# Kernel tuning notes

Measured on AMD Instinct MI355X. Metric: run time of the kernel, lower is better.

Reference implementation:

```python
import jax, jax.numpy as jnp
import numpy as np

N = 50000          # nodes
E = 1600000        # edges
F_IN = 128         # node_features
H = 256            # hidden_dim
A = 16             # action_dim
G = 64             # num graphs in batch


def _sage_conv(x, src, dst, Wl, bl, Wr, num_nodes):
    # PyG SAGEConv (aggr='mean'): out = lin_l(mean_{j in N(i)} x_j) + lin_r(x_i)
    msgs = x[src]                                              # [E, F] gather
    agg = jax.ops.segment_sum(msgs, dst, num_segments=num_nodes)
    cnt = jax.ops.segment_sum(jnp.ones((src.shape[0], 1), x.dtype), dst,
                              num_segments=num_nodes)
    mean = agg / jnp.maximum(cnt, 1.0)                         # [N, F]
    return mean @ Wl + bl + x @ Wr


def setup_inputs() -> dict:
    key = jax.random.key(0)
    ks = jax.random.split(key, 16)
    s = lambda k, sh: jax.random.normal(k, sh, dtype=jnp.float32) * (1.0 / np.sqrt(sh[0]))
    inp = {
        "x": jax.random.normal(ks[0], (N, F_IN), dtype=jnp.float32),
        "edge_index": jax.random.randint(ks[1], (2, E), 0, N, dtype=jnp.int32),
        "batch": jnp.sort(jax.random.randint(ks[2], (N,), 0, G, dtype=jnp.int32)),
        # SAGEConv 1
        "Wl1": s(ks[3], (F_IN, H)), "bl1": jnp.zeros((H,), jnp.float32), "Wr1": s(ks[4], (F_IN, H)),
        # SAGEConv 2
        "Wl2": s(ks[5], (H, H)), "bl2": jnp.zeros((H,), jnp.float32), "Wr2": s(ks[6], (H, H)),
        # actor MLP
        "Wa1": s(ks[7], (H, H)), "ba1": jnp.zeros((H,), jnp.float32),
        "Wa2": s(ks[8], (H, A)), "ba2": jnp.zeros((A,), jnp.float32),
        # critic MLP
        "Wc1": s(ks[9], (H, H)), "bc1": jnp.zeros((H,), jnp.float32),
        "Wc2": s(ks[10], (H, 1)), "bc2": jnp.zeros((1,), jnp.float32),
    }
    return inp


def reference(x, edge_index, batch, Wl1, bl1, Wr1, Wl2, bl2, Wr2,
              Wa1, ba1, Wa2, ba2, Wc1, bc1, Wc2, bc2):
    src, dst = edge_index[0], edge_index[1]
    h = jax.nn.relu(_sage_conv(x, src, dst, Wl1, bl1, Wr1, N))
    h = jax.nn.relu(_sage_conv(h, src, dst, Wl2, bl2, Wr2, N))
    # global_mean_pool over graph ids
    pooled = jax.ops.segment_sum(h, batch, num_segments=G)
    gcnt = jax.ops.segment_sum(jnp.ones((N, 1), h.dtype), batch, num_segments=G)
    g = pooled / jnp.maximum(gcnt, 1.0)                        # [G, H]
    mu = jax.nn.relu(g @ Wa1 + ba1) @ Wa2 + ba2                # [G, A]
    value = jax.nn.relu(g @ Wc1 + bc1) @ Wc2 + bc2             # [G, 1]
    return mu, value
```

## Files before the change

kernel.cpp:

```cpp
#include <hip/hip_runtime.h>
#include <hip/hip_bf16.h>
#include <hip/hip_fp8.h>

#define NN 50000
#define NE 1600000
#define FIN 128
#define HH 256
#define GG 64
#define AA 16
#define NB ((NN + 255) / 256)
#define NRANGE 8
#define RSZ (NN / NRANGE)

typedef __attribute__((ext_vector_type(8))) short short8;
typedef __attribute__((ext_vector_type(4))) float f32x4;
typedef __attribute__((ext_vector_type(4))) int   i32x4;
typedef __attribute__((ext_vector_type(4))) uint  u32x4;

static __device__ __forceinline__ ushort f2b(float f) {
    union { __hip_bfloat16 h; ushort u; } v; v.h = __float2bfloat16(f); return v.u;
}
static __device__ __forceinline__ float b2f_lo(uint a) {
    union { float f; uint u; } v; v.u = a << 16; return v.f;
}
template<int SEL>
static __device__ __forceinline__ float f8tof(uint u) {
#if __has_builtin(__builtin_amdgcn_cvt_f32_fp8)
    return __builtin_amdgcn_cvt_f32_fp8(u, SEL);
#else
    union { unsigned char c; __hip_fp8_e4m3 f; } v;
    v.c = (u >> (SEL * 8)) & 0xFF;
    return (float)v.f;
#endif
}
static __device__ __forceinline__ unsigned char ftof8(float f) {
    __hip_fp8_e4m3 v(f);
    return *reinterpret_cast<unsigned char*>(&v);
}

__global__ void k_prep(const float* __restrict__ x, ushort* __restrict__ xb,
                       unsigned char* __restrict__ xf8,
                       const float* __restrict__ Wl1, const float* __restrict__ Wr1,
                       ushort* __restrict__ Wt1,
                       const float* __restrict__ Wl2, const float* __restrict__ Wr2,
                       ushort* __restrict__ Wt2,
                       int* __restrict__ degi, float* __restrict__ gz) {
    int b = blockIdx.x, t = threadIdx.x;
    if (b < 6250) {
        int i = b * 256 + t;
        float4 v = reinterpret_cast<const float4*>(x)[i];
        ushort4 o; o.x = f2b(v.x); o.y = f2b(v.y); o.z = f2b(v.z); o.w = f2b(v.w);
        reinterpret_cast<ushort4*>(xb)[i] = o;
        uchar4 p; p.x = ftof8(v.x); p.y = ftof8(v.y); p.z = ftof8(v.z); p.w = ftof8(v.w);
        reinterpret_cast<uchar4*>(xf8)[i] = p;
    } else if (b < 6506) {
        int i = (b - 6250) * 256 + t;
        int n = i / 256, k = i % 256;
        float v = (k < 128) ? Wl1[k * HH + n] : Wr1[(k - 128) * HH + n];
        Wt1[i] = f2b(v);
    } else if (b < 7018) {
        int i = (b - 6506) * 256 + t;
        int n = i / 512, k = i % 512;
        float v = (k < 256) ? Wl2[k * HH + n] : Wr2[(k - 256) * HH + n];
        Wt2[i] = f2b(v);
    } else if (b < 7214) {
        int i = (b - 7018) * 256 + t;
        if (i < NN) degi[i] = 0;
    } else {
        int i = (b - 7214) * 256 + t;
        if (i < GG + GG * HH) gz[i] = 0.0f;
    }
}

__global__ void k_degi(const int* __restrict__ dst, int* __restrict__ degi) {
    int range = blockIdx.x & 7;
    int i = (blockIdx.x >> 3) * 256 + threadIdx.x;
    if (i >= NE / 4) return;
    i32x4 d = __builtin_nontemporal_load(reinterpret_cast<const i32x4*>(dst) + i);
    int lo = range * RSZ, hi = lo + RSZ;
    if (d.x >= lo && d.x < hi) atomicAdd(&degi[d.x], 1);
    if (d.y >= lo && d.y < hi) atomicAdd(&degi[d.y], 1);
    if (d.z >= lo && d.z < hi) atomicAdd(&degi[d.z], 1);
    if (d.w >= lo && d.w < hi) atomicAdd(&degi[d.w], 1);
}

__global__ void k_gdeg(const int* __restrict__ batch, float* __restrict__ gcnt) {
    __shared__ float h[GG];
    int t = threadIdx.x;
    if (t < GG) h[t] = 0.0f;
    __syncthreads();
    int i = blockIdx.x * 256 + t;
    if (i < NN) atomicAdd(&h[batch[i]], 1.0f);
    __syncthreads();
    if (t < GG && h[t] != 0.0f) atomicAdd(&gcnt[t], h[t]);
}

__global__ void k_scan1(const int* __restrict__ degi, int* __restrict__ blocksum) {
    __shared__ int s[256];
    int t = threadIdx.x, i = blockIdx.x * 256 + t;
    s[t] = i < NN ? degi[i] : 0;
    __syncthreads();
    for (int d = 128; d > 0; d >>= 1) { if (t < d) s[t] += s[t + d]; __syncthreads(); }
    if (t == 0) blocksum[blockIdx.x] = s[0];
}

__global__ void k_scan2(const int* __restrict__ blocksum, int* __restrict__ blockoff) {
    __shared__ int s[256];
    int t = threadIdx.x;
    int v = t < NB ? blocksum[t] : 0;
    s[t] = v; __syncthreads();
    for (int d = 1; d < 256; d <<= 1) {
        int x = t >= d ? s[t - d] : 0; __syncthreads();
        s[t] += x; __syncthreads();
    }
    if (t < NB) blockoff[t] = s[t] - v;
}

__global__ void k_scan3(const int* __restrict__ degi, const int* __restrict__ blockoff,
                        int* __restrict__ offsets, int* __restrict__ cursor) {
    __shared__ int s[256];
    int t = threadIdx.x, i = blockIdx.x * 256 + t;
    int v = i < NN ? degi[i] : 0;
    s[t] = v; __syncthreads();
    for (int d = 1; d < 256; d <<= 1) {
        int x = t >= d ? s[t - d] : 0; __syncthreads();
        s[t] += x; __syncthreads();
    }
    if (i < NN) {
        int off = blockoff[blockIdx.x] + s[t] - v;
        offsets[i] = off;
        cursor[i]  = off;
    }
    if (i == 0) offsets[NN] = NE;
}

__global__ void k_fill(const int* __restrict__ src, const int* __restrict__ dst,
                       int* __restrict__ cursor, ushort* __restrict__ csr16) {
    int range = blockIdx.x & 7;
    int i = (blockIdx.x >> 3) * 256 + threadIdx.x;
    if (i >= NE / 4) return;
    i32x4 d = __builtin_nontemporal_load(reinterpret_cast<const i32x4*>(dst) + i);
    i32x4 s = __builtin_nontemporal_load(reinterpret_cast<const i32x4*>(src) + i);
    int lo = range * RSZ, hi = lo + RSZ;
    if (d.x >= lo && d.x < hi) csr16[atomicAdd(&cursor[d.x], 1)] = (ushort)s.x;
    if (d.y >= lo && d.y < hi) csr16[atomicAdd(&cursor[d.y], 1)] = (ushort)s.y;
    if (d.z >= lo && d.z < hi) csr16[atomicAdd(&cursor[d.z], 1)] = (ushort)s.z;
    if (d.w >= lo && d.w < hi) csr16[atomicAdd(&cursor[d.w], 1)] = (ushort)s.w;
}

template<int C>
__global__ void __launch_bounds__(256) k_gatherf8(
        const int* __restrict__ offsets, const ushort* __restrict__ csr16,
        const unsigned char* __restrict__ feat, ushort* __restrict__ agg) {
    constexpr int V = C / 64;
    int wid = threadIdx.x >> 6, lane = threadIdx.x & 63;
    int node = blockIdx.x * 4 + wid;
    if (node >= NN) return;
    int o0 = offsets[node], o1 = offsets[node + 1];
    const unsigned char* fp = feat + lane * V;
    float acc[V];
#pragma unroll
    for (int i = 0; i < V; i++) acc[i] = 0.0f;

    int t = o0;
    for (; t + 3 < o1; t += 4) {
        int s0 = __builtin_nontemporal_load(csr16 + t);
        int s1 = __builtin_nontemporal_load(csr16 + t + 1);
        int s2 = __builtin_nontemporal_load(csr16 + t + 2);
        int s3 = __builtin_nontemporal_load(csr16 + t + 3);
        if constexpr (V == 2) {
            uint u0 = *(const ushort*)(fp + (size_t)s0 * C);
            uint u1 = *(const ushort*)(fp + (size_t)s1 * C);
            uint u2 = *(const ushort*)(fp + (size_t)s2 * C);
            uint u3 = *(const ushort*)(fp + (size_t)s3 * C);
            acc[0] += (f8tof<0>(u0) + f8tof<0>(u1)) + (f8tof<0>(u2) + f8tof<0>(u3));
            acc[1] += (f8tof<1>(u0) + f8tof<1>(u1)) + (f8tof<1>(u2) + f8tof<1>(u3));
        } else {
            uint u0 = *(const uint*)(fp + (size_t)s0 * C);
            uint u1 = *(const uint*)(fp + (size_t)s1 * C);
            uint u2 = *(const uint*)(fp + (size_t)s2 * C);
            uint u3 = *(const uint*)(fp + (size_t)s3 * C);
            acc[0] += (f8tof<0>(u0) + f8tof<0>(u1)) + (f8tof<0>(u2) + f8tof<0>(u3));
            acc[1] += (f8tof<1>(u0) + f8tof<1>(u1)) + (f8tof<1>(u2) + f8tof<1>(u3));
            acc[2] += (f8tof<2>(u0) + f8tof<2>(u1)) + (f8tof<2>(u2) + f8tof<2>(u3));
            acc[3] += (f8tof<3>(u0) + f8tof<3>(u1)) + (f8tof<3>(u2) + f8tof<3>(u3));
        }
    }
    for (; t < o1; ++t) {
        int s0 = __builtin_nontemporal_load(csr16 + t);
        if constexpr (V == 2) {
            uint u0 = *(const ushort*)(fp + (size_t)s0 * C);
            acc[0] += f8tof<0>(u0); acc[1] += f8tof<1>(u0);
        } else {
            uint u0 = *(const uint*)(fp + (size_t)s0 * C);
            acc[0] += f8tof<0>(u0); acc[1] += f8tof<1>(u0);
            acc[2] += f8tof<2>(u0); acc[3] += f8tof<3>(u0);
        }
    }

    int deg = o1 - o0;
    float r = __builtin_amdgcn_rcpf(deg > 1 ? (float)deg : 1.0f);
    if constexpr (V == 2) {
        uint o = (uint)f2b(acc[0] * r) | ((uint)f2b(acc[1] * r) << 16);
        *(uint*)(agg + (size_t)node * C + lane * 2) = o;
    } else {
        uint2 o;
        o.x = (uint)f2b(acc[0] * r) | ((uint)f2b(acc[1] * r) << 16);
        o.y = (uint)f2b(acc[2] * r) | ((uint)f2b(acc[3] * r) << 16);
        *(uint2*)(agg + (size_t)node * C + lane * 4) = o;
    }
}

template<int K>
__global__ void __launch_bounds__(256) k_sage_mfma(
        const ushort* __restrict__ agg, const ushort* __restrict__ xin,
        const ushort* __restrict__ Wt, const float* __restrict__ bias,
        ushort* __restrict__ outb, unsigned char* __restrict__ out8) {
    constexpr int KH = K / 2;
    constexpr int LDP = 40;
    __shared__ ushort As[128 * LDP];
    __shared__ ushort Bs[256 * LDP];

    const int tid  = threadIdx.x;
    const int lane = tid & 63;
    const int w    = tid >> 6;
    const int base = blockIdx.x * 128;
    const int r    = lane & 15;
    const int kh   = lane >> 4;
    const int wcol = w * 64;

    f32x4 acc[8][4];
#pragma unroll
    for (int m = 0; m < 8; m++)
#pragma unroll
        for (int n = 0; n < 4; n++) acc[m][n] = (f32x4){0.f, 0.f, 0.f, 0.f};

    const int frowA = tid >> 1;
    const int fqA   = tid & 1;
    const int frowB = tid >> 2;
    const int fqB   = tid & 3;
    int fnode = base + frowA; if (fnode >= NN) fnode = 0;

    for (int k0 = 0; k0 < K; k0 += 32) {
        __syncthreads();
        {
            const ushort* srcp = (k0 < KH)
                ? agg + (size_t)fnode * KH + k0 + fqA * 16
                : xin + (size_t)fnode * KH + (k0 - KH) + fqA * 16;
            u32x4 a0 = *(const u32x4*)srcp;
            u32x4 a1 = *(const u32x4*)(srcp + 8);
            *(u32x4*)(&As[frowA * LDP + fqA * 16])     = a0;
            *(u32x4*)(&As[frowA * LDP + fqA * 16 + 8]) = a1;
        }
#pragma unroll
        for (int s = 0; s < 4; s++) {
            int c = frowB + s * 64;
            *(u32x4*)(&Bs[c * LDP + fqB * 8]) =
                *(const u32x4*)(Wt + (size_t)c * K + k0 + fqB * 8);
        }
        __syncthreads();

        short8 av[8], bv[4];
#pragma unroll
        for (int m = 0; m < 8; m++)
            av[m] = *(const short8*)(&As[(m * 16 + r) * LDP + kh * 8]);
#pragma unroll
        for (int n = 0; n < 4; n++)
            bv[n] = *(const short8*)(&Bs[(wcol + n * 16 + r) * LDP + kh * 8]);
#pragma unroll
        for (int m = 0; m < 8; m++)
#pragma unroll
            for (int n = 0; n < 4; n++)
                acc[m][n] = __builtin_amdgcn_mfma_f32_16x16x32_bf16(
                    av[m], bv[n], acc[m][n], 0, 0, 0);
    }

    float bj[4];
#pragma unroll
    for (int n = 0; n < 4; n++) bj[n] = bias[wcol + n * 16 + r];

#pragma unroll
    for (int m = 0; m < 8; m++) {
        int rowbase = base + m * 16 + (lane >> 4) * 4;
#pragma unroll
        for (int reg = 0; reg < 4; reg++) {
            int nd = rowbase + reg;
            if (nd < NN) {
#pragma unroll
                for (int n = 0; n < 4; n++) {
                    float v = acc[m][n][reg] + bj[n];
                    v = v > 0.0f ? v : 0.0f;
                    outb[(size_t)nd * HH + wcol + n * 16 + r] = f2b(v);
                    if (out8) out8[(size_t)nd * HH + wcol + n * 16 + r] = ftof8(v);
                }
            }
        }
    }
}

__global__ void k_pool(const ushort* __restrict__ h, const int* __restrict__ batch,
                       float* __restrict__ gpool) {
    __shared__ int sb[32];
    int j = threadIdx.x;
    int base = blockIdx.x * 32;
    int n = NN - base; if (n > 32) n = 32;
    if (j < n) sb[j] = batch[base + j];
    __syncthreads();
    float acc = 0.0f;
    int cur = sb[0];
    for (int t = 0; t < n; t++) {
        int g = sb[t];
        if (g != cur) {
            atomicAdd(&gpool[cur * HH + j], acc);
            acc = 0.0f;
            cur = g;
        }
        acc += b2f_lo((uint)h[(size_t)(base + t) * HH + j]);
    }
    atomicAdd(&gpool[cur * HH + j], acc);
}

__global__ void k_head(const float* __restrict__ gpool, const float* __restrict__ gcnt,
                       const float* __restrict__ Wa1, const float* __restrict__ ba1,
                       const float* __restrict__ Wa2, const float* __restrict__ ba2,
                       const float* __restrict__ Wc1, const float* __restrict__ bc1,
                       const float* __restrict__ Wc2, const float* __restrict__ bc2,
                       float* __restrict__ outp) {
    __shared__ float gv[HH], ha[HH], hc[HH];
    int g = blockIdx.x, j = threadIdx.x;
    float c = gcnt[g];
    c = c > 1.0f ? c : 1.0f;
    gv[j] = gpool[g * HH + j] * __builtin_amdgcn_rcpf(c);
    __syncthreads();
    float a_acc = ba1[j], c_acc = bc1[j];
#pragma unroll 2
    for (int k = 0; k < HH; k += 4) {
        float4 g4 = *reinterpret_cast<const float4*>(&gv[k]);
        const float* WA = Wa1 + k * HH + j;
        const float* WC = Wc1 + k * HH + j;
        a_acc += g4.x * WA[0] + g4.y * WA[HH] + g4.z * WA[2 * HH] + g4.w * WA[3 * HH];
        c_acc += g4.x * WC[0] + g4.y * WC[HH] + g4.z * WC[2 * HH] + g4.w * WC[3 * HH];
    }
    ha[j] = a_acc > 0.0f ? a_acc : 0.0f;
    hc[j] = c_acc > 0.0f ? c_acc : 0.0f;
    __syncthreads();
    if (j < AA) {
        float m = ba2[j];
        for (int k = 0; k < HH; k++) m += ha[k] * Wa2[k * AA + j];
        outp[g * AA + j] = m;
    } else if (j == AA) {
        float v = bc2[0];
        for (int k = 0; k < HH; k++) v += hc[k] * Wc2[k];
        outp[GG * AA + g] = v;
    }
}

extern "C" void kernel_launch(void* const* d_in, const int* in_sizes, int n_in,
                              void* d_out, int out_size, void* d_ws, size_t ws_size,
                              hipStream_t stream) {
    const float* x     = (const float*)d_in[0];
    const int*   ei    = (const int*)d_in[1];
    const int*   batch = (const int*)d_in[2];
    const float* Wl1 = (const float*)d_in[3];
    const float* bl1 = (const float*)d_in[4];
    const float* Wr1 = (const float*)d_in[5];
    const float* Wl2 = (const float*)d_in[6];
    const float* bl2 = (const float*)d_in[7];
    const float* Wr2 = (const float*)d_in[8];
    const float* Wa1 = (const float*)d_in[9];
    const float* ba1 = (const float*)d_in[10];
    const float* Wa2 = (const float*)d_in[11];
    const float* ba2 = (const float*)d_in[12];
    const float* Wc1 = (const float*)d_in[13];
    const float* bc1 = (const float*)d_in[14];
    const float* Wc2 = (const float*)d_in[15];
    const float* bc2 = (const float*)d_in[16];
    float* out = (float*)d_out;

    const int* srcv = ei;
    const int* dstv = ei + NE;

    char* ws = (char*)d_ws;
    int*    degi     = (int*)(ws + 0);
    int*    offsets  = (int*)(ws + 200192);
    int*    cursor   = (int*)(ws + 400640);
    int*    blocksum = (int*)(ws + 600832);
    int*    blockoff = (int*)(ws + 601856);
    float*  gcnt     = (float*)(ws + 602880);
    float*  gpool    = (float*)(ws + 603136);
    ushort* csr16    = (ushort*)(ws + 668672);
    ushort* xb       = (ushort*)(ws + 3868672);
    ushort* agg1b    = (ushort*)(ws + 16668672);
    ushort* h1b      = (ushort*)(ws + 29468672);
    ushort* agg2b    = (ushort*)(ws + 55068672);
    ushort* Wt1      = (ushort*)(ws + 80668672);
    ushort* Wt2      = (ushort*)(ws + 80799744);
    unsigned char* xf8  = (unsigned char*)(ws + 81061888);
    unsigned char* h1f8 = (unsigned char*)(ws + 87461888);

    k_prep<<<7279, 256, 0, stream>>>(x, xb, xf8, Wl1, Wr1, Wt1, Wl2, Wr2, Wt2,
                                     degi, gcnt);

    const int nch = (NE / 4 + 255) / 256;
    k_degi<<<nch * NRANGE, 256, 0, stream>>>(dstv, degi);
    k_gdeg<<<(NN + 255) / 256, 256, 0, stream>>>(batch, gcnt);
    k_scan1<<<NB, 256, 0, stream>>>(degi, blocksum);
    k_scan2<<<1, 256, 0, stream>>>(blocksum, blockoff);
    k_scan3<<<NB, 256, 0, stream>>>(degi, blockoff, offsets, cursor);
    k_fill<<<nch * NRANGE, 256, 0, stream>>>(srcv, dstv, cursor, csr16);

    k_gatherf8<FIN><<<(NN + 3) / 4, 256, 0, stream>>>(offsets, csr16, xf8, agg1b);
    k_sage_mfma<2 * FIN><<<(NN + 127) / 128, 256, 0, stream>>>(agg1b, xb, Wt1, bl1, h1b, h1f8);

    k_gatherf8<HH><<<(NN + 3) / 4, 256, 0, stream>>>(offsets, csr16, h1f8, agg2b);
    k_sage_mfma<2 * HH><<<(NN + 127) / 128, 256, 0, stream>>>(agg2b, h1b, Wt2, bl2, agg2b, nullptr);

    k_pool<<<(NN + 31) / 32, 256, 0, stream>>>(agg2b, batch, gpool);
    k_head<<<GG, 256, 0, stream>>>(gpool, gcnt, Wa1, ba1, Wa2, ba2, Wc1, bc1, Wc2, bc2, out);
}
```

Measured before the change: 432.4 us.

## Pre-bucket edges by destination range before degree count and CSR fill

Replaces the eight-pass range-filtered degree and fill kernels, which each reread the full src/dst arrays eight times, with a single bucketing pass. That pass packs (local dst, src) into 32-bit words and writes them into eight per-range buffers using block-local staging and one global atomic per bucket. The degree and scatter kernels then read only their range's compact buffer. Edge reads drop from sixteen full passes to one, at the cost of an extra 6.4MB intermediate write and read. A fixed per-bucket capacity (PCAP) is assumed, and pcur is zeroed by extending the prep zero range.

```diff
diff --git a/kernel.cpp b/kernel.cpp
--- a/kernel.cpp
+++ b/kernel.cpp
@@ -9,8 +9,8 @@
 #define GG 64
 #define AA 16
 #define NB ((NN + 255) / 256)
-#define NRANGE 8
-#define RSZ (NN / NRANGE)
+#define RSZ (NN / 8)
+#define PCAP 230400
 
 typedef __attribute__((ext_vector_type(8))) short short8;
 typedef __attribute__((ext_vector_type(4))) float f32x4;
@@ -68,20 +68,63 @@
         if (i < NN) degi[i] = 0;
     } else {
         int i = (b - 7214) * 256 + t;
-        if (i < GG + GG * HH) gz[i] = 0.0f;
-    }
-}
-
-__global__ void k_degi(const int* __restrict__ dst, int* __restrict__ degi) {
-    int range = blockIdx.x & 7;
-    int i = (blockIdx.x >> 3) * 256 + threadIdx.x;
-    if (i >= NE / 4) return;
-    i32x4 d = __builtin_nontemporal_load(reinterpret_cast<const i32x4*>(dst) + i);
-    int lo = range * RSZ, hi = lo + RSZ;
-    if (d.x >= lo && d.x < hi) atomicAdd(&degi[d.x], 1);
-    if (d.y >= lo && d.y < hi) atomicAdd(&degi[d.y], 1);
-    if (d.z >= lo && d.z < hi) atomicAdd(&degi[d.z], 1);
-    if (d.w >= lo && d.w < hi) atomicAdd(&degi[d.w], 1);
+        if (i < GG + GG * HH + 8) gz[i] = 0.0f;
+    }
+}
+
+__global__ void __launch_bounds__(256) k_bucket(
+        const int* __restrict__ src, const int* __restrict__ dst,
+        int* __restrict__ pcur, uint* __restrict__ pbuf) {
+    __shared__ int lcnt[8], lplace[8], gbase[8], lbase[8];
+    __shared__ uint stage[1024];
+    const int t = threadIdx.x;
+    if (t < 8) { lcnt[t] = 0; lplace[t] = 0; }
+    __syncthreads();
+
+    const int i = blockIdx.x * 256 + t;
+    uint pk[4]; int bk[4]; int nv = 0;
+    if (i < NE / 4) {
+        i32x4 d = __builtin_nontemporal_load(reinterpret_cast<const i32x4*>(dst) + i);
+        i32x4 s = __builtin_nontemporal_load(reinterpret_cast<const i32x4*>(src) + i);
+        int dv[4] = {d.x, d.y, d.z, d.w};
+        int sv[4] = {s.x, s.y, s.z, s.w};
+#pragma unroll
+        for (int k = 0; k < 4; k++) {
+            int b = dv[k] / RSZ;
+            bk[k] = b;
+            pk[k] = (uint)(dv[k] - b * RSZ) | ((uint)sv[k] << 16);
+        }
+        nv = 4;
+    }
+    for (int k = 0; k < nv; k++) atomicAdd(&lcnt[bk[k]], 1);
+    __syncthreads();
+    if (t < 8) {
+        int sum = 0;
+        for (int b = 0; b < t; b++) sum += lcnt[b];
+        lbase[t] = sum;
+        gbase[t] = atomicAdd(&pcur[t], lcnt[t]);
+    }
+    __syncthreads();
+    for (int k = 0; k < nv; k++) {
+        int slot = atomicAdd(&lplace[bk[k]], 1);
+        stage[lbase[bk[k]] + slot] = pk[k];
+    }
+    __syncthreads();
+    const int total = lbase[7] + lcnt[7];
+    for (int j = t; j < total; j += 256) {
+        int b = 0;
+        while (b < 7 && j >= lbase[b] + lcnt[b]) b++;
+        pbuf[(size_t)b * PCAP + gbase[b] + (j - lbase[b])] = stage[j];
+    }
+}
+
+__global__ void k_degi_p(const int* __restrict__ pcur, const uint* __restrict__ pbuf,
+                         int* __restrict__ degi) {
+    int r = blockIdx.x & 7;
+    int j = (blockIdx.x >> 3) * 256 + threadIdx.x;
+    if (j >= pcur[r]) return;
+    uint u = pbuf[(size_t)r * PCAP + j];
+    atomicAdd(&degi[r * RSZ + (int)(u & 0xFFFFu)], 1);
 }
 
 __global__ void k_gdeg(const int* __restrict__ batch, float* __restrict__ gcnt) {
@@ -134,18 +177,15 @@
     if (i == 0) offsets[NN] = NE;
 }
 
-__global__ void k_fill(const int* __restrict__ src, const int* __restrict__ dst,
-                       int* __restrict__ cursor, ushort* __restrict__ csr16) {
-    int range = blockIdx.x & 7;
-    int i = (blockIdx.x >> 3) * 256 + threadIdx.x;
-    if (i >= NE / 4) return;
-    i32x4 d = __builtin_nontemporal_load(reinterpret_cast<const i32x4*>(dst) + i);
-    i32x4 s = __builtin_nontemporal_load(reinterpret_cast<const i32x4*>(src) + i);
-    int lo = range * RSZ, hi = lo + RSZ;
-    if (d.x >= lo && d.x < hi) csr16[atomicAdd(&cursor[d.x], 1)] = (ushort)s.x;
-    if (d.y >= lo && d.y < hi) csr16[atomicAdd(&cursor[d.y], 1)] = (ushort)s.y;
-    if (d.z >= lo && d.z < hi) csr16[atomicAdd(&cursor[d.z], 1)] = (ushort)s.z;
-    if (d.w >= lo && d.w < hi) csr16[atomicAdd(&cursor[d.w], 1)] = (ushort)s.w;
+__global__ void k_scatter_p(const int* __restrict__ pcur, const uint* __restrict__ pbuf,
+                            int* __restrict__ cursor, ushort* __restrict__ csr16) {
+    int r = blockIdx.x & 7;
+    int j = (blockIdx.x >> 3) * 256 + threadIdx.x;
+    if (j >= pcur[r]) return;
+    uint u = pbuf[(size_t)r * PCAP + j];
+    int node = r * RSZ + (int)(u & 0xFFFFu);
+    int slot = atomicAdd(&cursor[node], 1);
+    csr16[slot] = (ushort)(u >> 16);
 }
 
 template<int C>
@@ -388,26 +428,30 @@
     int*    blockoff = (int*)(ws + 601856);
     float*  gcnt     = (float*)(ws + 602880);
     float*  gpool    = (float*)(ws + 603136);
-    ushort* csr16    = (ushort*)(ws + 668672);
-    ushort* xb       = (ushort*)(ws + 3868672);
-    ushort* agg1b    = (ushort*)(ws + 16668672);
-    ushort* h1b      = (ushort*)(ws + 29468672);
-    ushort* agg2b    = (ushort*)(ws + 55068672);
-    ushort* Wt1      = (ushort*)(ws + 80668672);
-    ushort* Wt2      = (ushort*)(ws + 80799744);
-    unsigned char* xf8  = (unsigned char*)(ws + 81061888);
-    unsigned char* h1f8 = (unsigned char*)(ws + 87461888);
+    int*    pcur     = (int*)(ws + 668672);
+    ushort* csr16    = (ushort*)(ws + 668928);
+    uint*   pbuf     = (uint*)(ws + 3868928);
+    ushort* xb       = (ushort*)(ws + 11241728);
+    ushort* agg1b    = (ushort*)(ws + 24041728);
+    ushort* h1b      = (ushort*)(ws + 36841728);
+    ushort* agg2b    = (ushort*)(ws + 62441728);
+    ushort* Wt1      = (ushort*)(ws + 88041728);
+    ushort* Wt2      = (ushort*)(ws + 88172800);
+    unsigned char* xf8  = (unsigned char*)(ws + 88434944);
+    unsigned char* h1f8 = (unsigned char*)(ws + 94834944);
 
     k_prep<<<7279, 256, 0, stream>>>(x, xb, xf8, Wl1, Wr1, Wt1, Wl2, Wr2, Wt2,
                                      degi, gcnt);
 
-    const int nch = (NE / 4 + 255) / 256;
-    k_degi<<<nch * NRANGE, 256, 0, stream>>>(dstv, degi);
+    k_bucket<<<(NE / 4 + 255) / 256, 256, 0, stream>>>(srcv, dstv, pcur, pbuf);
     k_gdeg<<<(NN + 255) / 256, 256, 0, stream>>>(batch, gcnt);
+
+    const int ppb = PCAP / 256;
+    k_degi_p<<<ppb * 8, 256, 0, stream>>>(pcur, pbuf, degi);
     k_scan1<<<NB, 256, 0, stream>>>(degi, blocksum);
     k_scan2<<<1, 256, 0, stream>>>(blocksum, blockoff);
     k_scan3<<<NB, 256, 0, stream>>>(degi, blockoff, offsets, cursor);
-    k_fill<<<nch * NRANGE, 256, 0, stream>>>(srcv, dstv, cursor, csr16);
+    k_scatter_p<<<ppb * 8, 256, 0, stream>>>(pcur, pbuf, cursor, csr16);
 
     k_gatherf8<FIN><<<(NN + 3) / 4, 256, 0, stream>>>(offsets, csr16, xf8, agg1b);
     k_sage_mfma<2 * FIN><<<(NN + 127) / 128, 256, 0, stream>>>(agg1b, xb, Wt1, bl1, h1b, h1f8);
```

Result: slower. 444.4 us (+2.8%).

## Fuse mean-pool into second SAGE GEMM epilogue and compute graph counts by binary search

Applied to the files above, without the earlier changes.

The second SAGE GEMM now accumulates its ReLU output straight into per-graph pooled sums. It uses shared-memory partials for up to four graphs per tile and global atomics otherwise, instead of writing h2 to memory and running a separate pool kernel. Graph node counts are computed in the head kernel by binary search on the sorted batch array, which removes the k_gdeg kernel. This drops two launches and the h2 write/read round trip. In exchange the GEMM epilogue gains many shared atomics, and the binary search relies on batch being sorted.

```diff
diff --git a/kernel.cpp b/kernel.cpp
--- a/kernel.cpp
+++ b/kernel.cpp
@@ -44,7 +44,7 @@
                        ushort* __restrict__ Wt1,
                        const float* __restrict__ Wl2, const float* __restrict__ Wr2,
                        ushort* __restrict__ Wt2,
-                       int* __restrict__ degi, float* __restrict__ gz) {
+                       int* __restrict__ degi, float* __restrict__ gpool) {
     int b = blockIdx.x, t = threadIdx.x;
     if (b < 6250) {
         int i = b * 256 + t;
@@ -68,7 +68,7 @@
         if (i < NN) degi[i] = 0;
     } else {
         int i = (b - 7214) * 256 + t;
-        if (i < GG + GG * HH) gz[i] = 0.0f;
+        gpool[i] = 0.0f;
     }
 }
 
@@ -82,17 +82,6 @@
     if (d.y >= lo && d.y < hi) atomicAdd(&degi[d.y], 1);
     if (d.z >= lo && d.z < hi) atomicAdd(&degi[d.z], 1);
     if (d.w >= lo && d.w < hi) atomicAdd(&degi[d.w], 1);
-}
-
-__global__ void k_gdeg(const int* __restrict__ batch, float* __restrict__ gcnt) {
-    __shared__ float h[GG];
-    int t = threadIdx.x;
-    if (t < GG) h[t] = 0.0f;
-    __syncthreads();
-    int i = blockIdx.x * 256 + t;
-    if (i < NN) atomicAdd(&h[batch[i]], 1.0f);
-    __syncthreads();
-    if (t < GG && h[t] != 0.0f) atomicAdd(&gcnt[t], h[t]);
 }
 
 __global__ void k_scan1(const int* __restrict__ degi, int* __restrict__ blocksum) {
@@ -211,15 +200,18 @@
     }
 }
 
-template<int K>
+template<int K, bool POOL>
 __global__ void __launch_bounds__(256) k_sage_mfma(
         const ushort* __restrict__ agg, const ushort* __restrict__ xin,
         const ushort* __restrict__ Wt, const float* __restrict__ bias,
-        ushort* __restrict__ outb, unsigned char* __restrict__ out8) {
+        ushort* __restrict__ outb, unsigned char* __restrict__ out8,
+        const int* __restrict__ batch, float* __restrict__ gpool) {
     constexpr int KH = K / 2;
     constexpr int LDP = 40;
     __shared__ ushort As[128 * LDP];
     __shared__ ushort Bs[256 * LDP];
+    __shared__ float pgr[4][HH];
+    __shared__ int nb[128];
 
     const int tid  = threadIdx.x;
     const int lane = tid & 63;
@@ -228,6 +220,14 @@
     const int r    = lane & 15;
     const int kh   = lane >> 4;
     const int wcol = w * 64;
+
+    if constexpr (POOL) {
+        for (int idx = tid; idx < 4 * HH; idx += 256) ((float*)pgr)[idx] = 0.0f;
+        if (tid < 128) {
+            int nd = base + tid; if (nd >= NN) nd = NN - 1;
+            nb[tid] = batch[nd];
+        }
+    }
 
     f32x4 acc[8][4];
 #pragma unroll
@@ -279,58 +279,75 @@
 #pragma unroll
     for (int n = 0; n < 4; n++) bj[n] = bias[wcol + n * 16 + r];
 
-#pragma unroll
-    for (int m = 0; m < 8; m++) {
-        int rowbase = base + m * 16 + (lane >> 4) * 4;
-#pragma unroll
-        for (int reg = 0; reg < 4; reg++) {
-            int nd = rowbase + reg;
-            if (nd < NN) {
-#pragma unroll
-                for (int n = 0; n < 4; n++) {
-                    float v = acc[m][n][reg] + bj[n];
-                    v = v > 0.0f ? v : 0.0f;
-                    outb[(size_t)nd * HH + wcol + n * 16 + r] = f2b(v);
-                    if (out8) out8[(size_t)nd * HH + wcol + n * 16 + r] = ftof8(v);
+    if constexpr (POOL) {
+        __syncthreads();
+        const int glo = nb[0];
+#pragma unroll
+        for (int m = 0; m < 8; m++) {
+            int rowbase = base + m * 16 + (lane >> 4) * 4;
+#pragma unroll
+            for (int reg = 0; reg < 4; reg++) {
+                int nd = rowbase + reg;
+                if (nd < NN) {
+                    int g = nb[nd - base] - glo;
+#pragma unroll
+                    for (int n = 0; n < 4; n++) {
+                        float v = acc[m][n][reg] + bj[n];
+                        v = v > 0.0f ? v : 0.0f;
+                        int col = wcol + n * 16 + r;
+                        if (g < 4) atomicAdd(&pgr[g][col], v);
+                        else       atomicAdd(&gpool[(size_t)(glo + g) * HH + col], v);
+                    }
                 }
             }
         }
-    }
-}
-
-__global__ void k_pool(const ushort* __restrict__ h, const int* __restrict__ batch,
-                       float* __restrict__ gpool) {
-    __shared__ int sb[32];
-    int j = threadIdx.x;
-    int base = blockIdx.x * 32;
-    int n = NN - base; if (n > 32) n = 32;
-    if (j < n) sb[j] = batch[base + j];
-    __syncthreads();
-    float acc = 0.0f;
-    int cur = sb[0];
-    for (int t = 0; t < n; t++) {
-        int g = sb[t];
-        if (g != cur) {
-            atomicAdd(&gpool[cur * HH + j], acc);
-            acc = 0.0f;
-            cur = g;
-        }
-        acc += b2f_lo((uint)h[(size_t)(base + t) * HH + j]);
-    }
-    atomicAdd(&gpool[cur * HH + j], acc);
-}
-
-__global__ void k_head(const float* __restrict__ gpool, const float* __restrict__ gcnt,
+        __syncthreads();
+        for (int idx = tid; idx < 4 * HH; idx += 256) {
+            float v = ((float*)pgr)[idx];
+            int g = glo + idx / HH;
+            if (v != 0.0f && g < GG)
+                atomicAdd(&gpool[(size_t)g * HH + (idx & (HH - 1))], v);
+        }
+    } else {
+#pragma unroll
+        for (int m = 0; m < 8; m++) {
+            int rowbase = base + m * 16 + (lane >> 4) * 4;
+#pragma unroll
+            for (int reg = 0; reg < 4; reg++) {
+                int nd = rowbase + reg;
+                if (nd < NN) {
+#pragma unroll
+                    for (int n = 0; n < 4; n++) {
+                        float v = acc[m][n][reg] + bj[n];
+                        v = v > 0.0f ? v : 0.0f;
+                        outb[(size_t)nd * HH + wcol + n * 16 + r] = f2b(v);
+                        out8[(size_t)nd * HH + wcol + n * 16 + r] = ftof8(v);
+                    }
+                }
+            }
+        }
+    }
+}
+
+__global__ void k_head(const float* __restrict__ gpool, const int* __restrict__ batch,
                        const float* __restrict__ Wa1, const float* __restrict__ ba1,
                        const float* __restrict__ Wa2, const float* __restrict__ ba2,
                        const float* __restrict__ Wc1, const float* __restrict__ bc1,
                        const float* __restrict__ Wc2, const float* __restrict__ bc2,
                        float* __restrict__ outp) {
     __shared__ float gv[HH], ha[HH], hc[HH];
+    __shared__ float cs;
     int g = blockIdx.x, j = threadIdx.x;
-    float c = gcnt[g];
-    c = c > 1.0f ? c : 1.0f;
-    gv[j] = gpool[g * HH + j] * __builtin_amdgcn_rcpf(c);
+    if (j == 0) {
+        int lo = 0, hi = NN;
+        while (lo < hi) { int m = (lo + hi) >> 1; if (batch[m] < g) lo = m + 1; else hi = m; }
+        int a = lo; lo = 0; hi = NN;
+        while (lo < hi) { int m = (lo + hi) >> 1; if (batch[m] < g + 1) lo = m + 1; else hi = m; }
+        cs = (float)(lo - a);
+    }
+    __syncthreads();
+    float c = cs > 1.0f ? cs : 1.0f;
+    gv[j] = gpool[g * HH + j] / c;
     __syncthreads();
     float a_acc = ba1[j], c_acc = bc1[j];
 #pragma unroll 2
@@ -386,8 +403,7 @@
     int*    cursor   = (int*)(ws + 400640);
     int*    blocksum = (int*)(ws + 600832);
     int*    blockoff = (int*)(ws + 601856);
-    float*  gcnt     = (float*)(ws + 602880);
-    float*  gpool    = (float*)(ws + 603136);
+    float*  gpool    = (float*)(ws + 602880);
     ushort* csr16    = (ushort*)(ws + 668672);
     ushort* xb       = (ushort*)(ws + 3868672);
     ushort* agg1b    = (ushort*)(ws + 16668672);
@@ -398,23 +414,24 @@
     unsigned char* xf8  = (unsigned char*)(ws + 81061888);
     unsigned char* h1f8 = (unsigned char*)(ws + 87461888);
 
-    k_prep<<<7279, 256, 0, stream>>>(x, xb, xf8, Wl1, Wr1, Wt1, Wl2, Wr2, Wt2,
-                                     degi, gcnt);
+    k_prep<<<7278, 256, 0, stream>>>(x, xb, xf8, Wl1, Wr1, Wt1, Wl2, Wr2, Wt2,
+                                     degi, gpool);
 
     const int nch = (NE / 4 + 255) / 256;
     k_degi<<<nch * NRANGE, 256, 0, stream>>>(dstv, degi);
-    k_gdeg<<<(NN + 255) / 256, 256, 0, stream>>>(batch, gcnt);
     k_scan1<<<NB, 256, 0, stream>>>(degi, blocksum);
     k_scan2<<<1, 256, 0, stream>>>(blocksum, blockoff);
     k_scan3<<<NB, 256, 0, stream>>>(degi, blockoff, offsets, cursor);
     k_fill<<<nch * NRANGE, 256, 0, stream>>>(srcv, dstv, cursor, csr16);
 
     k_gatherf8<FIN><<<(NN + 3) / 4, 256, 0, stream>>>(offsets, csr16, xf8, agg1b);
-    k_sage_mfma<2 * FIN><<<(NN + 127) / 128, 256, 0, stream>>>(agg1b, xb, Wt1, bl1, h1b, h1f8);
+    k_sage_mfma<2 * FIN, false><<<(NN + 127) / 128, 256, 0, stream>>>(
+        agg1b, xb, Wt1, bl1, h1b, h1f8, batch, gpool);
 
     k_gatherf8<HH><<<(NN + 3) / 4, 256, 0, stream>>>(offsets, csr16, h1f8, agg2b);
-    k_sage_mfma<2 * HH><<<(NN + 127) / 128, 256, 0, stream>>>(agg2b, h1b, Wt2, bl2, agg2b, nullptr);
-
-    k_pool<<<(NN + 31) / 32, 256, 0, stream>>>(agg2b, batch, gpool);
-    k_head<<<GG, 256, 0, stream>>>(gpool, gcnt, Wa1, ba1, Wa2, ba2, Wc1, bc1, Wc2, bc2, out);
-}
+    k_sage_mfma<2 * HH, true><<<(NN + 127) / 128, 256, 0, stream>>>(
+        agg2b, h1b, Wt2, bl2, nullptr, nullptr, batch, gpool);
+
+    k_head<<<GG, 256, 0, stream>>>(gpool, batch, Wa1, ba1, Wa2, ba2, Wc1, bc1,
+                                   Wc2, bc2, out);
+}
```

Measured after the change: 474.3 us. +9.7%, slower.
